# Kernel optimization log

Hardware: AMD Instinct MI355X
Metric: run time of the kernel (lower is better)

## Reference

```python
import jax, jax.numpy as jnp
import numpy as np

N_EMBD = 768
N_HEAD = 12
HEAD_DIM = N_EMBD // N_HEAD
EPS = 1e-5


def _ln(x, g, b):
    mu = jnp.mean(x, axis=-1, keepdims=True)
    var = jnp.mean(jnp.square(x - mu), axis=-1, keepdims=True)
    return (x - mu) * jax.lax.rsqrt(var + EPS) * g + b


def _gelu(x):
    # GPT-2 / BERT tanh-approximate GELU (new_gelu)
    c = jnp.sqrt(2.0 / jnp.pi).astype(x.dtype)
    return 0.5 * x * (1.0 + jnp.tanh(c * (x + 0.044715 * x * x * x)))


def setup_inputs() -> dict:
    key = jax.random.key(0)
    ks = jax.random.split(key, 8)
    B, T, C = 4, 2048, N_EMBD
    s = 0.02
    return {
        "x": jax.random.normal(ks[0], (B, T, C), jnp.float32),
        "attention_mask": jnp.ones((B, T), jnp.float32),
        "ln1_g": jnp.ones((C,), jnp.float32),
        "ln1_b": jnp.zeros((C,), jnp.float32),
        "ln2_g": jnp.ones((C,), jnp.float32),
        "ln2_b": jnp.zeros((C,), jnp.float32),
        "W_attn": jax.random.normal(ks[1], (C, 3 * C), jnp.float32) * s,
        "b_attn": jnp.zeros((3 * C,), jnp.float32),
        "W_proj": jax.random.normal(ks[2], (C, C), jnp.float32) * s,
        "b_proj": jnp.zeros((C,), jnp.float32),
        "W_fc": jax.random.normal(ks[3], (C, 4 * C), jnp.float32) * s,
        "b_fc": jnp.zeros((4 * C,), jnp.float32),
        "W_out": jax.random.normal(ks[4], (4 * C, C), jnp.float32) * s,
        "b_out": jnp.zeros((C,), jnp.float32),
    }


def reference(x, attention_mask, ln1_g, ln1_b, ln2_g, ln2_b,
              W_attn, b_attn, W_proj, b_proj, W_fc, b_fc, W_out, b_out):
    B, T, C = x.shape
    H, D = N_HEAD, HEAD_DIM

    # --- attention sublayer ---
    h = _ln(x, ln1_g, ln1_b)
    qkv = h @ W_attn + b_attn                      # [B,T,3C]
    q, k, v = jnp.split(qkv, 3, axis=-1)
    q = q.reshape(B, T, H, D).transpose(0, 2, 1, 3)  # [B,H,T,D]
    k = k.reshape(B, T, H, D).transpose(0, 2, 1, 3)
    v = v.reshape(B, T, H, D).transpose(0, 2, 1, 3)

    att = jnp.einsum('bhqd,bhkd->bhqk', q, k) * (1.0 / jnp.sqrt(D).astype(x.dtype))
    mask_add = (1.0 - attention_mask)[:, None, None, :] * -10000.0  # [B,1,1,T]
    att = att + mask_add
    att = jax.nn.softmax(att, axis=-1)
    y = jnp.einsum('bhqk,bhkd->bhqd', att, v)      # [B,H,T,D]
    y = y.transpose(0, 2, 1, 3).reshape(B, T, C)
    x = x + (y @ W_proj + b_proj)

    # --- MLP sublayer ---
    h = _ln(x, ln2_g, ln2_b)
    h = _gelu(h @ W_fc + b_fc)
    x = x + (h @ W_out + b_out)
    return x
```

## Files before the change

kernel.cpp:

```cpp
#include <hip/hip_runtime.h>
#include <hip/hip_bf16.h>
#include <cstdint>

using short8   = __attribute__((ext_vector_type(8))) short;
using floatx4  = __attribute__((ext_vector_type(4))) float;
using float2v  = __attribute__((ext_vector_type(2))) float;
using ushort4v = __attribute__((ext_vector_type(4))) unsigned short;

#define DEVI static __device__ __forceinline__

DEVI unsigned short f2bf(float f) {
    union { float f; unsigned u; } v; v.f = f;
    unsigned r = v.u + 0x7FFFu + ((v.u >> 16) & 1u);
    return (unsigned short)(r >> 16);
}

DEVI unsigned cvtpk_bf16(float lo, float hi) {
    unsigned r;
    asm("v_cvt_pk_bf16_f32 %0, %1, %2" : "=v"(r) : "v"(lo), "v"(hi));
    return r;
}

typedef const __attribute__((address_space(1))) unsigned int gas_uint;
typedef __attribute__((address_space(3))) unsigned int las_uint;

DEVI void gload16(const void* g, void* l) {
    __builtin_amdgcn_global_load_lds((gas_uint*)g, (las_uint*)l, 16, 0, 0);
}

DEVI float gelu_f(float x) {
    float z = 0.7978845608028654f * (x + 0.044715f * x * x * x);
    float e = __expf(2.0f * z);
    float t = 1.0f - 2.0f / (e + 1.0f);
    return 0.5f * x * (1.0f + t);
}

DEVI int xcd_swizzle(int gX) {
    const int nwg = gX * gridDim.y;
    const int orig = blockIdx.y * gX + blockIdx.x;
    if (nwg & 7) return orig;
    return (orig & 7) * (nwg >> 3) + (orig >> 3);
}

#define QSCALE 0.18033688011112042f

__global__ __launch_bounds__(256)
void transpose_cast(const float* __restrict__ W, unsigned short* __restrict__ Wt,
                    int K, int N)
{
    __shared__ float tile[32][33];
    const int n0 = blockIdx.x * 32, k0 = blockIdx.y * 32;
    const int tx = threadIdx.x & 31, ty = threadIdx.x >> 5;
#pragma unroll
    for (int j = 0; j < 4; ++j)
        tile[ty + j * 8][tx] = W[(long)(k0 + ty + j * 8) * N + n0 + tx];
    __syncthreads();
#pragma unroll
    for (int j = 0; j < 4; ++j)
        Wt[(long)(n0 + ty + j * 8) * K + k0 + tx] = f2bf(tile[tx][ty + j * 8]);
}

__global__ __launch_bounds__(256)
void ln_cast_k(const float* __restrict__ x, const float* __restrict__ g,
               const float* __restrict__ beta, unsigned short* __restrict__ out)
{
    const int row = blockIdx.x;
    const int tid = threadIdx.x;
    const float* xr = x + (long)row * 768;
    float v0 = xr[tid], v1 = xr[tid + 256], v2 = xr[tid + 512];
    float s  = v0 + v1 + v2;
    float sq = v0 * v0 + v1 * v1 + v2 * v2;
#pragma unroll
    for (int m = 1; m < 64; m <<= 1) {
        s  += __shfl_xor(s, m);
        sq += __shfl_xor(sq, m);
    }
    __shared__ float ss[4], ssq[4];
    if ((tid & 63) == 0) { ss[tid >> 6] = s; ssq[tid >> 6] = sq; }
    __syncthreads();
    s  = ss[0] + ss[1] + ss[2] + ss[3];
    sq = ssq[0] + ssq[1] + ssq[2] + ssq[3];
    const float mean = s * (1.0f / 768.0f);
    const float var  = sq * (1.0f / 768.0f) - mean * mean;
    const float rstd = rsqrtf(var + 1e-5f);
    unsigned short* orow = out + (long)row * 768;
    orow[tid]       = f2bf((v0 - mean) * rstd * g[tid]       + beta[tid]);
    orow[tid + 256] = f2bf((v1 - mean) * rstd * g[tid + 256] + beta[tid + 256]);
    orow[tid + 512] = f2bf((v2 - mean) * rstd * g[tid + 512] + beta[tid + 512]);
}

template<int EPI>
__global__ __launch_bounds__(256)
void gemm128(const unsigned short* __restrict__ A,
             const unsigned short* __restrict__ Bt,
             const float* __restrict__ bias,
             unsigned short* __restrict__ ob0,
             unsigned short* __restrict__ ob1,
             unsigned short* __restrict__ ob2,
             int K, int N)
{
    const int wg = xcd_swizzle(gridDim.x);
    const int gY = gridDim.y;
    const int mt = wg / gY, nt = wg % gY;
    const int tid = threadIdx.x;
    const int w = tid >> 6, lane = tid & 63;
    const int l16 = lane & 15, lq = lane >> 4;
    const int wm = w >> 1, wn = w & 1;

    __shared__ unsigned short As[128 * 64];
    __shared__ unsigned short Bs[128 * 64];

    const floatx4 fzero = {0.f, 0.f, 0.f, 0.f};
    floatx4 acc[4][4];
#pragma unroll
    for (int i = 0; i < 4; ++i)
#pragma unroll
        for (int j = 0; j < 4; ++j) acc[i][j] = fzero;

    const char* Abyte = (const char*)A + (long)mt * 128 * K * 2;
    const char* Bbyte = (const char*)Bt + (long)nt * 128 * K * 2;
    const int KT = K >> 6;

    for (int kt = 0; kt < KT; ++kt) {
        const int kbyte = kt * 128;
#pragma unroll
        for (int r4 = 0; r4 < 4; ++r4) {
            int base = (w * 4 + r4) * 1024;
            int loff = base + lane * 16;
            int row  = loff >> 7;
            int scb  = (loff & 127) ^ ((row & 7) << 4);
            gload16(Abyte + (long)row * (K * 2) + kbyte + scb, (char*)As + base);
            gload16(Bbyte + (long)row * (K * 2) + kbyte + scb, (char*)Bs + base);
        }
        __syncthreads();
#pragma unroll
        for (int ks = 0; ks < 2; ++ks) {
            const int kb = ks * 64 + lq * 16;
            short8 af[4], bfr[4];
#pragma unroll
            for (int f = 0; f < 4; ++f) {
                int ar = wm * 64 + f * 16 + l16;
                af[f]  = *(const short8*)((const char*)As + ar * 128 + (kb ^ ((ar & 7) << 4)));
                int br = wn * 64 + f * 16 + l16;
                bfr[f] = *(const short8*)((const char*)Bs + br * 128 + (kb ^ ((br & 7) << 4)));
            }
#pragma unroll
            for (int i = 0; i < 4; ++i)
#pragma unroll
                for (int j = 0; j < 4; ++j)
                    acc[i][j] = __builtin_amdgcn_mfma_f32_16x16x32_bf16(af[i], bfr[j], acc[i][j], 0, 0, 0);
        }
        __syncthreads();
    }

    const int col0 = nt * 128 + wn * 64;
    const int row0 = mt * 128 + wm * 64;
#pragma unroll
    for (int j = 0; j < 4; ++j) {
        const int col = col0 + j * 16 + l16;
        const float bv = bias[col];
#pragma unroll
        for (int i = 0; i < 4; ++i) {
            const int rowb = row0 + i * 16 + lq * 4;
            float v[4];
#pragma unroll
            for (int r = 0; r < 4; ++r) v[r] = acc[i][j][r] + bv;

            if (EPI == 0) {
                const int which = (col >= 1536) ? 2 : (col >= 768 ? 1 : 0);
                const int c = col - which * 768;
                const int hh = c >> 6, d = c & 63;
                const int bb = rowb >> 11;
                const int t  = rowb & 2047;
                if (which == 2) {
                    ushort4v pk;
#pragma unroll
                    for (int r = 0; r < 4; ++r) pk[r] = f2bf(v[r]);
                    const int tlo = t & 31;
                    const int tS  = (t & ~31) + ((tlo & 12) << 1) + ((tlo & 16) >> 2);
                    long vi = ((long)(bb * 12 + hh) * 64 + d) * 2048 + tS;
                    *(ushort4v*)(ob2 + vi) = pk;
                } else {
                    unsigned short* dst = (which == 0) ? ob0 : ob1;
                    const float qs = (which == 0) ? QSCALE : 1.0f;
                    long base = ((long)(bb * 12 + hh) * 2048 + t) * 64 + d;
#pragma unroll
                    for (int r = 0; r < 4; ++r) dst[base + (long)r * 64] = f2bf(v[r] * qs);
                }
            } else {
#pragma unroll
                for (int r = 0; r < 4; ++r) {
                    long idx = (long)(rowb + r) * N + col;
                    ob0[idx] = f2bf(gelu_f(v[r]));
                }
            }
        }
    }
}

__global__ __launch_bounds__(256)
void gemm_n64(const unsigned short* __restrict__ A,
              const unsigned short* __restrict__ Bt,
              const float* __restrict__ bias,
              const float* __restrict__ resid,
              float* __restrict__ of,
              int K, int N)
{
    const int wg = xcd_swizzle(gridDim.x);
    const int gY = gridDim.y;
    const int mt = wg / gY, nt = wg % gY;
    const int tid = threadIdx.x;
    const int w = tid >> 6, lane = tid & 63;
    const int l16 = lane & 15, lq = lane >> 4;
    const int wm = w >> 1, wn = w & 1;

    __shared__ unsigned short As[128 * 64];
    __shared__ unsigned short Bs[64 * 64];

    const floatx4 fzero = {0.f, 0.f, 0.f, 0.f};
    floatx4 acc[4][2];
#pragma unroll
    for (int i = 0; i < 4; ++i)
#pragma unroll
        for (int j = 0; j < 2; ++j) acc[i][j] = fzero;

    const int K2 = K * 2;
    const char* Abyte = (const char*)A + (long)mt * 128 * K2;
    const char* Bbyte = (const char*)Bt + (long)nt * 64 * K2;
    const int KT = K >> 6;

    for (int kt = 0; kt < KT; ++kt) {
        const int kbyte = kt * 128;
#pragma unroll
        for (int r4 = 0; r4 < 4; ++r4) {
            int base = (w * 4 + r4) * 1024;
            int loff = base + lane * 16;
            int row  = loff >> 7;
            int scb  = (loff & 127) ^ ((row & 7) << 4);
            gload16(Abyte + (long)row * K2 + kbyte + scb, (char*)As + base);
        }
#pragma unroll
        for (int r2 = 0; r2 < 2; ++r2) {
            int base = (w * 2 + r2) * 1024;
            int loff = base + lane * 16;
            int row  = loff >> 7;
            int scb  = (loff & 127) ^ ((row & 7) << 4);
            gload16(Bbyte + (long)row * K2 + kbyte + scb, (char*)Bs + base);
        }
        __syncthreads();
#pragma unroll
        for (int ks = 0; ks < 2; ++ks) {
            const int kb = ks * 64 + lq * 16;
            short8 af[4], bfr[2];
#pragma unroll
            for (int f = 0; f < 4; ++f) {
                int ar = wm * 64 + f * 16 + l16;
                af[f] = *(const short8*)((const char*)As + ar * 128 + (kb ^ ((ar & 7) << 4)));
            }
#pragma unroll
            for (int f = 0; f < 2; ++f) {
                int br = wn * 32 + f * 16 + l16;
                bfr[f] = *(const short8*)((const char*)Bs + br * 128 + (kb ^ ((br & 7) << 4)));
            }
#pragma unroll
            for (int i = 0; i < 4; ++i)
#pragma unroll
                for (int j = 0; j < 2; ++j)
                    acc[i][j] = __builtin_amdgcn_mfma_f32_16x16x32_bf16(af[i], bfr[j], acc[i][j], 0, 0, 0);
        }
        __syncthreads();
    }

    const int col0 = nt * 64 + wn * 32;
    const int row0 = mt * 128 + wm * 64;
#pragma unroll
    for (int j = 0; j < 2; ++j) {
        const int col = col0 + j * 16 + l16;
        const float bv = bias[col];
#pragma unroll
        for (int i = 0; i < 4; ++i) {
            const int rowb = row0 + i * 16 + lq * 4;
#pragma unroll
            for (int r = 0; r < 4; ++r) {
                long idx = (long)(rowb + r) * N + col;
                of[idx] = acc[i][j][r] + bv + resid[idx];
            }
        }
    }
}

__global__ __launch_bounds__(512)
void attn_fwd(const unsigned short* __restrict__ q,
              const unsigned short* __restrict__ k,
              const unsigned short* __restrict__ vt,
              const float* __restrict__ mask,
              unsigned short* __restrict__ y)
{
    const int qt = blockIdx.x;
    const int bh = blockIdx.y;
    const int b = bh / 12, h = bh - b * 12;
    const int tid = threadIdx.x;
    const int w = tid >> 6, lane = tid & 63;
    const int l16 = lane & 15, lq = lane >> 4;

    __shared__ unsigned short Ks[128 * 64];
    __shared__ unsigned short Vs[64 * 128];
    __shared__ float madd[128];
    __shared__ int mq;

    if (tid == 0) mq = 0;
    __syncthreads();
    {
        const float* mrow = mask + (long)b * 2048 + tid * 4;
        int bad = 0;
#pragma unroll
        for (int j = 0; j < 4; ++j) bad |= (mrow[j] != 1.0f);
        if (bad) atomicOr(&mq, 1);
    }

    const unsigned short* qrow = q + ((long)bh * 2048 + qt * 128 + w * 16 + l16) * 64;
    const short8 qf0 = *(const short8*)(qrow + lq * 8);
    const short8 qf1 = *(const short8*)(qrow + 32 + lq * 8);

    const char* kg = (const char*)(k + (long)bh * 2048 * 64);
    const char* vg = (const char*)(vt + (long)bh * 64 * 2048);
    int koff[2], voff[2], lb[2];
#pragma unroll
    for (int r2 = 0; r2 < 2; ++r2) {
        int loff = r2 * 8192 + tid * 16;
        int rowK = loff >> 7;
        koff[r2] = rowK * 128 + ((loff & 127) ^ ((rowK & 7) << 4));
        int rowV = loff >> 8;
        voff[r2] = rowV * 4096 + ((loff & 255) ^ ((rowV & 7) << 4));
        lb[r2]   = loff;
    }

    __syncthreads();
    const bool usemask = (mq != 0);

    const floatx4 fzero = {0.f, 0.f, 0.f, 0.f};
    floatx4 accO[4];
#pragma unroll
    for (int n = 0; n < 4; ++n) accO[n] = fzero;
    float m2 = -1e30f, lsum = 0.f;

    for (int kt = 0; kt < 16; ++kt) {
        const char* kgt = kg + (long)kt * 16384;
        const char* vgt = vg + kt * 256;
#pragma unroll
        for (int r2 = 0; r2 < 2; ++r2) {
            gload16(kgt + koff[r2], (char*)Ks + lb[r2]);
            gload16(vgt + voff[r2], (char*)Vs + lb[r2]);
        }
        if (usemask && tid < 128)
            madd[tid] = (1.0f - mask[b * 2048 + kt * 128 + tid]) * (-10000.0f * 1.4426950408889634f);
        __syncthreads();

        floatx4 st[8];
#pragma unroll
        for (int f = 0; f < 8; ++f) st[f] = fzero;
        __builtin_amdgcn_s_setprio(1);
#pragma unroll
        for (int f = 0; f < 8; ++f) {
            const int kr = f * 16 + l16;
            const int sw = (kr & 7) << 4;
            short8 ka0 = *(const short8*)((const char*)Ks + kr * 128 + ((lq * 16) ^ sw));
            short8 ka1 = *(const short8*)((const char*)Ks + kr * 128 + ((64 + lq * 16) ^ sw));
            st[f] = __builtin_amdgcn_mfma_f32_16x16x32_bf16(ka0, qf0, st[f], 0, 0, 0);
            st[f] = __builtin_amdgcn_mfma_f32_16x16x32_bf16(ka1, qf1, st[f], 0, 0, 0);
        }
        __builtin_amdgcn_s_setprio(0);

        if (usemask) {
#pragma unroll
            for (int f = 0; f < 8; ++f) {
                floatx4 md = *(const floatx4*)((const char*)madd + f * 64 + lq * 16);
                st[f] += md;
            }
        }

        float2v lo[8], hi[8];
#pragma unroll
        for (int f = 0; f < 8; ++f) {
            lo[f][0] = st[f][0]; lo[f][1] = st[f][1];
            hi[f][0] = st[f][2]; hi[f][1] = st[f][3];
        }

        float2v mx = __builtin_elementwise_max(lo[0], hi[0]);
#pragma unroll
        for (int f = 1; f < 8; ++f)
            mx = __builtin_elementwise_max(mx, __builtin_elementwise_max(lo[f], hi[f]));
        float rm = fmaxf(mx[0], mx[1]);
        rm = fmaxf(rm, __shfl_xor(rm, 16));
        rm = fmaxf(rm, __shfl_xor(rm, 32));

        if (!__all(rm <= m2 + 8.0f)) {
            const float mn = fmaxf(m2, rm);
            const float corr = exp2f(m2 - mn);
            m2 = mn;
            lsum *= corr;
            floatx4 cv;
            cv[0] = __shfl(corr, lq * 4 + 0);
            cv[1] = __shfl(corr, lq * 4 + 1);
            cv[2] = __shfl(corr, lq * 4 + 2);
            cv[3] = __shfl(corr, lq * 4 + 3);
#pragma unroll
            for (int n = 0; n < 4; ++n) accO[n] *= cv;
        }

        const float2v m2v = {m2, m2};
        float2v rs2 = {0.f, 0.f};
        unsigned pw[16];
#pragma unroll
        for (int f = 0; f < 8; ++f) {
            float2v d0 = lo[f] - m2v;
            float2v d1 = hi[f] - m2v;
            float2v e0, e1;
            e0[0] = exp2f(d0[0]); e0[1] = exp2f(d0[1]);
            e1[0] = exp2f(d1[0]); e1[1] = exp2f(d1[1]);
            rs2 += e0;
            rs2 += e1;
            pw[f * 2]     = cvtpk_bf16(e0[0], e0[1]);
            pw[f * 2 + 1] = cvtpk_bf16(e1[0], e1[1]);
        }
        float rs = rs2[0] + rs2[1];
        rs += __shfl_xor(rs, 16);
        rs += __shfl_xor(rs, 32);
        lsum += rs;

        __builtin_amdgcn_s_setprio(1);
#pragma unroll
        for (int c = 0; c < 4; ++c) {
            union { unsigned u[4]; short8 s8; } pu;
            pu.u[0] = pw[c * 4 + 0];
            pu.u[1] = pw[c * 4 + 1];
            pu.u[2] = pw[c * 4 + 2];
            pu.u[3] = pw[c * 4 + 3];
            const int kb2 = c * 64 + lq * 16;
#pragma unroll
            for (int n = 0; n < 4; ++n) {
                const int vr = n * 16 + l16;
                short8 vb = *(const short8*)((const char*)Vs + vr * 256 + (kb2 ^ ((vr & 7) << 4)));
                accO[n] = __builtin_amdgcn_mfma_f32_16x16x32_bf16(pu.s8, vb, accO[n], 0, 0, 0);
            }
        }
        __builtin_amdgcn_s_setprio(0);
        __syncthreads();
    }

    const float li = 1.0f / lsum;
    floatx4 lv;
    lv[0] = __shfl(li, lq * 4 + 0);
    lv[1] = __shfl(li, lq * 4 + 1);
    lv[2] = __shfl(li, lq * 4 + 2);
    lv[3] = __shfl(li, lq * 4 + 3);
    unsigned short* ybase = y + ((long)(b * 2048 + qt * 128 + w * 16 + lq * 4)) * 768 + h * 64;
#pragma unroll
    for (int r = 0; r < 4; ++r) {
        unsigned short* yrow = ybase + (long)r * 768;
#pragma unroll
        for (int n = 0; n < 4; ++n)
            yrow[n * 16 + l16] = f2bf(accO[n][r] * lv[r]);
    }
}

extern "C" void kernel_launch(void* const* d_in, const int* in_sizes, int n_in,
                              void* d_out, int out_size, void* d_ws, size_t ws_size,
                              hipStream_t stream)
{
    const float* x     = (const float*)d_in[0];
    const float* amask = (const float*)d_in[1];
    const float* ln1g  = (const float*)d_in[2];
    const float* ln1b  = (const float*)d_in[3];
    const float* ln2g  = (const float*)d_in[4];
    const float* ln2b  = (const float*)d_in[5];
    const float* Wattn = (const float*)d_in[6];
    const float* battn = (const float*)d_in[7];
    const float* Wproj = (const float*)d_in[8];
    const float* bproj = (const float*)d_in[9];
    const float* Wfc   = (const float*)d_in[10];
    const float* bfc   = (const float*)d_in[11];
    const float* Wout  = (const float*)d_in[12];
    const float* bout  = (const float*)d_in[13];
    float* out = (float*)d_out;

    char* ws = (char*)d_ws;
    unsigned short* wt_attn = (unsigned short*)ws;  ws += (long)2304 * 768 * 2;
    unsigned short* wt_proj = (unsigned short*)ws;  ws += (long)768 * 768 * 2;
    unsigned short* wt_fc   = (unsigned short*)ws;  ws += (long)3072 * 768 * 2;
    unsigned short* wt_out  = (unsigned short*)ws;  ws += (long)768 * 3072 * 2;
    unsigned short* hbuf    = (unsigned short*)ws;  ws += (long)8192 * 768 * 2;
    unsigned short* qbuf    = (unsigned short*)ws;  ws += (long)48 * 2048 * 64 * 2;
    unsigned short* kbuf    = (unsigned short*)ws;  ws += (long)48 * 2048 * 64 * 2;
    unsigned short* vtbuf   = (unsigned short*)ws;  ws += (long)48 * 2048 * 64 * 2;
    unsigned short* ybuf    = (unsigned short*)ws;  ws += (long)8192 * 768 * 2;
    unsigned short* hfc     = (unsigned short*)ws;  ws += (long)8192 * 3072 * 2;

    transpose_cast<<<dim3(2304 / 32, 768 / 32), 256, 0, stream>>>(Wattn, wt_attn, 768, 2304);
    transpose_cast<<<dim3(768 / 32, 768 / 32), 256, 0, stream>>>(Wproj, wt_proj, 768, 768);
    transpose_cast<<<dim3(3072 / 32, 768 / 32), 256, 0, stream>>>(Wfc, wt_fc, 768, 3072);
    transpose_cast<<<dim3(768 / 32, 3072 / 32), 256, 0, stream>>>(Wout, wt_out, 3072, 768);

    ln_cast_k<<<8192, 256, 0, stream>>>(x, ln1g, ln1b, hbuf);

    gemm128<0><<<dim3(64, 18), 256, 0, stream>>>(hbuf, wt_attn, battn,
                                                 qbuf, kbuf, vtbuf, 768, 2304);

    attn_fwd<<<dim3(16, 48), 512, 0, stream>>>(qbuf, kbuf, vtbuf, amask, ybuf);

    gemm_n64<<<dim3(64, 12), 256, 0, stream>>>(ybuf, wt_proj, bproj, x, out, 768, 768);

    ln_cast_k<<<8192, 256, 0, stream>>>(out, ln2g, ln2b, hbuf);

    gemm128<2><<<dim3(64, 24), 256, 0, stream>>>(hbuf, wt_fc, bfc,
                                                 hfc, nullptr, nullptr, 768, 3072);

    gemm_n64<<<dim3(64, 12), 256, 0, stream>>>(hfc, wt_out, bout, out, out, 3072, 768);
}
```

Before: 318.4 us.

## Double-buffer K tiles in attention and merge weight transpose launches

```diff
diff --git a/kernel.cpp b/kernel.cpp
--- a/kernel.cpp
+++ b/kernel.cpp
@@ -26,6 +26,12 @@
 
 DEVI void gload16(const void* g, void* l) {
     __builtin_amdgcn_global_load_lds((gas_uint*)g, (las_uint*)l, 16, 0, 0);
+}
+
+DEVI void barrier_raw() {
+    asm volatile("" ::: "memory");
+    __builtin_amdgcn_s_barrier();
+    asm volatile("" ::: "memory");
 }
 
 DEVI float gelu_f(float x) {
@@ -45,19 +51,28 @@
 #define QSCALE 0.18033688011112042f
 
 __global__ __launch_bounds__(256)
-void transpose_cast(const float* __restrict__ W, unsigned short* __restrict__ Wt,
-                    int K, int N)
+void transpose_cast_all(const float* __restrict__ W0, const float* __restrict__ W1,
+                        const float* __restrict__ W2, const float* __restrict__ W3,
+                        unsigned short* __restrict__ T0, unsigned short* __restrict__ T1,
+                        unsigned short* __restrict__ T2, unsigned short* __restrict__ T3)
 {
-    __shared__ float tile[32][33];
-    const int n0 = blockIdx.x * 32, k0 = blockIdx.y * 32;
+    const int bid = blockIdx.x;
+    const float* W; unsigned short* Wt; int K, N, nx, tile;
+    if (bid < 1728)      { W = W0; Wt = T0; K = 768;  N = 2304; nx = 72; tile = bid; }
+    else if (bid < 2304) { W = W1; Wt = T1; K = 768;  N = 768;  nx = 24; tile = bid - 1728; }
+    else if (bid < 4608) { W = W2; Wt = T2; K = 768;  N = 3072; nx = 96; tile = bid - 2304; }
+    else                 { W = W3; Wt = T3; K = 3072; N = 768;  nx = 24; tile = bid - 4608; }
+    const int n0 = (tile % nx) * 32, k0 = (tile / nx) * 32;
+
+    __shared__ float tile_s[32][33];
     const int tx = threadIdx.x & 31, ty = threadIdx.x >> 5;
 #pragma unroll
     for (int j = 0; j < 4; ++j)
-        tile[ty + j * 8][tx] = W[(long)(k0 + ty + j * 8) * N + n0 + tx];
+        tile_s[ty + j * 8][tx] = W[(long)(k0 + ty + j * 8) * N + n0 + tx];
     __syncthreads();
 #pragma unroll
     for (int j = 0; j < 4; ++j)
-        Wt[(long)(n0 + ty + j * 8) * K + k0 + tx] = f2bf(tile[tx][ty + j * 8]);
+        Wt[(long)(n0 + ty + j * 8) * K + k0 + tx] = f2bf(tile_s[tx][ty + j * 8]);
 }
 
 __global__ __launch_bounds__(256)
@@ -303,9 +318,9 @@
     const int w = tid >> 6, lane = tid & 63;
     const int l16 = lane & 15, lq = lane >> 4;
 
-    __shared__ unsigned short Ks[128 * 64];
+    __shared__ unsigned short Ks[2][128 * 64];
     __shared__ unsigned short Vs[64 * 128];
-    __shared__ float madd[128];
+    __shared__ float madd[2][128];
     __shared__ int mq;
 
     if (tid == 0) mq = 0;
@@ -338,6 +353,17 @@
     __syncthreads();
     const bool usemask = (mq != 0);
 
+#pragma unroll
+    for (int r2 = 0; r2 < 2; ++r2)
+        gload16(kg + koff[r2], (char*)Ks[0] + lb[r2]);
+#pragma unroll
+    for (int r2 = 0; r2 < 2; ++r2)
+        gload16(vg + voff[r2], (char*)Vs + lb[r2]);
+    if (usemask && tid < 128)
+        madd[0][tid] = (1.0f - mask[b * 2048 + tid]) * (-10000.0f * 1.4426950408889634f);
+    asm volatile("s_waitcnt vmcnt(2)" ::: "memory");
+    barrier_raw();
+
     const floatx4 fzero = {0.f, 0.f, 0.f, 0.f};
     floatx4 accO[4];
 #pragma unroll
@@ -345,17 +371,18 @@
     float m2 = -1e30f, lsum = 0.f;
 
     for (int kt = 0; kt < 16; ++kt) {
-        const char* kgt = kg + (long)kt * 16384;
-        const char* vgt = vg + kt * 256;
-#pragma unroll
-        for (int r2 = 0; r2 < 2; ++r2) {
-            gload16(kgt + koff[r2], (char*)Ks + lb[r2]);
-            gload16(vgt + voff[r2], (char*)Vs + lb[r2]);
-        }
-        if (usemask && tid < 128)
-            madd[tid] = (1.0f - mask[b * 2048 + kt * 128 + tid]) * (-10000.0f * 1.4426950408889634f);
-        __syncthreads();
-
+        const int cur = kt & 1;
+
+        if (kt < 15) {
+            const char* kgt = kg + (long)(kt + 1) * 16384;
+#pragma unroll
+            for (int r2 = 0; r2 < 2; ++r2)
+                gload16(kgt + koff[r2], (char*)Ks[cur ^ 1] + lb[r2]);
+            if (usemask && tid < 128)
+                madd[cur ^ 1][tid] = (1.0f - mask[b * 2048 + (kt + 1) * 128 + tid]) * (-10000.0f * 1.4426950408889634f);
+        }
+
+        const char* Kc = (const char*)Ks[cur];
         floatx4 st[8];
 #pragma unroll
         for (int f = 0; f < 8; ++f) st[f] = fzero;
@@ -364,8 +391,8 @@
         for (int f = 0; f < 8; ++f) {
             const int kr = f * 16 + l16;
             const int sw = (kr & 7) << 4;
-            short8 ka0 = *(const short8*)((const char*)Ks + kr * 128 + ((lq * 16) ^ sw));
-            short8 ka1 = *(const short8*)((const char*)Ks + kr * 128 + ((64 + lq * 16) ^ sw));
+            short8 ka0 = *(const short8*)(Kc + kr * 128 + ((lq * 16) ^ sw));
+            short8 ka1 = *(const short8*)(Kc + kr * 128 + ((64 + lq * 16) ^ sw));
             st[f] = __builtin_amdgcn_mfma_f32_16x16x32_bf16(ka0, qf0, st[f], 0, 0, 0);
             st[f] = __builtin_amdgcn_mfma_f32_16x16x32_bf16(ka1, qf1, st[f], 0, 0, 0);
         }
@@ -374,7 +401,7 @@
         if (usemask) {
 #pragma unroll
             for (int f = 0; f < 8; ++f) {
-                floatx4 md = *(const floatx4*)((const char*)madd + f * 64 + lq * 16);
+                floatx4 md = *(const floatx4*)((const char*)madd[cur] + f * 64 + lq * 16);
                 st[f] += md;
             }
         }
@@ -385,7 +412,6 @@
             lo[f][0] = st[f][0]; lo[f][1] = st[f][1];
             hi[f][0] = st[f][2]; hi[f][1] = st[f][3];
         }
-
         float2v mx = __builtin_elementwise_max(lo[0], hi[0]);
 #pragma unroll
         for (int f = 1; f < 8; ++f)
@@ -428,6 +454,9 @@
         rs += __shfl_xor(rs, 32);
         lsum += rs;
 
+        asm volatile("s_waitcnt vmcnt(0)" ::: "memory");
+        barrier_raw();
+
         __builtin_amdgcn_s_setprio(1);
 #pragma unroll
         for (int c = 0; c < 4; ++c) {
@@ -445,7 +474,15 @@
             }
         }
         __builtin_amdgcn_s_setprio(0);
-        __syncthreads();
+
+        barrier_raw();
+
+        if (kt < 15) {
+            const char* vgt = vg + (kt + 1) * 256;
+#pragma unroll
+            for (int r2 = 0; r2 < 2; ++r2)
+                gload16(vgt + voff[r2], (char*)Vs + lb[r2]);
+        }
     }
 
     const float li = 1.0f / lsum;
@@ -496,10 +533,8 @@
     unsigned short* ybuf    = (unsigned short*)ws;  ws += (long)8192 * 768 * 2;
     unsigned short* hfc     = (unsigned short*)ws;  ws += (long)8192 * 3072 * 2;
 
-    transpose_cast<<<dim3(2304 / 32, 768 / 32), 256, 0, stream>>>(Wattn, wt_attn, 768, 2304);
-    transpose_cast<<<dim3(768 / 32, 768 / 32), 256, 0, stream>>>(Wproj, wt_proj, 768, 768);
-    transpose_cast<<<dim3(3072 / 32, 768 / 32), 256, 0, stream>>>(Wfc, wt_fc, 768, 3072);
-    transpose_cast<<<dim3(768 / 32, 3072 / 32), 256, 0, stream>>>(Wout, wt_out, 3072, 768);
+    transpose_cast_all<<<6912, 256, 0, stream>>>(Wattn, Wproj, Wfc, Wout,
+                                                 wt_attn, wt_proj, wt_fc, wt_out);
 
     ln_cast_k<<<8192, 256, 0, stream>>>(x, ln1g, ln1b, hbuf);
 
```

New measurement: 312.0 us. 2.0% less time.
